# Optimization experiments

Hardware: AMD Instinct MI355X
Metric: run time of the kernel (lower is better)

The kernel has to match this reference:

```python
import jax, jax.numpy as jnp
import numpy as np

B, N, IN, H, OUT = 128, 8192, 9, 128, 9


def setup_inputs() -> dict:
    key = jax.random.key(0)
    ks = jax.random.split(key, 4)
    y = jax.random.normal(ks[0], (B, N, 6), dtype=jnp.float32)
    W1 = jax.random.normal(ks[1], (IN, H), dtype=jnp.float32) / np.sqrt(IN)
    b1 = jnp.zeros((H,), dtype=jnp.float32)
    W2 = jax.random.normal(ks[2], (H, H), dtype=jnp.float32) / np.sqrt(H)
    b2 = jnp.zeros((H,), dtype=jnp.float32)
    W3 = jax.random.normal(ks[3], (H, OUT), dtype=jnp.float32) / np.sqrt(H)
    b3 = jnp.zeros((OUT,), dtype=jnp.float32)
    return {"y": y, "W1": W1, "b1": b1, "W2": W2, "b2": b2, "W3": W3, "b3": b3}


def _make_triplets(coords):
    # coords: (B, N, 3) -> (B, N-2, 9) = (a1, a2, a3, x1, y1, x2, y2, x3, y3)
    xp = coords[:, :-2, :]
    xm = coords[:, 1:-1, :]
    xn = coords[:, 2:, :]
    off = jnp.arctan2(xm[..., 1] - xp[..., 1], xm[..., 0] - xp[..., 0])
    return jnp.stack(
        (xp[..., 2] - off, xm[..., 2] - off, xn[..., 2] - off,
         xp[..., 0], xp[..., 1], xm[..., 0], xm[..., 1], xn[..., 0], xn[..., 1]),
        axis=-1,
    )


def reference(y, W1, b1, W2, b2, W3, b3):
    coords = y[..., :3]                      # (B, N, 3)
    t = _make_triplets(coords)               # (B, N-2, 9)
    h = jax.nn.swish(t @ W1 + b1)            # (B, N-2, H)
    h = jax.nn.swish(h @ W2 + b2)            # (B, N-2, H)
    f = h @ W3 + b3                          # (B, N-2, 9)
    # overlap-add scatter back onto the N cycles
    res = jnp.zeros_like(coords)
    res = res.at[:, :-2, :].add(jnp.stack([f[..., 3], f[..., 4], f[..., 0]], axis=-1))
    res = res.at[:, 1:-1, :].add(jnp.stack([f[..., 5], f[..., 6], f[..., 1]], axis=-1))
    res = res.at[:, 2:, :].add(jnp.stack([f[..., 7], f[..., 8], f[..., 2]], axis=-1))
    # boundaries = (1, 1): clamp both ends
    res = res.at[:, 0, :].set(0.0)
    res = res.at[:, -1, :].set(0.0)
    return res
```

## Files before the change

### kernel.cpp

```cpp
#include <hip/hip_runtime.h>
#include <hip/hip_bf16.h>

#define Bn 128
#define Nn 8192
#define Hn 128
#define RPB 128
#define JOUT 126
#define NBJ 66

typedef __attribute__((ext_vector_type(8))) short short8;
typedef __attribute__((ext_vector_type(4))) float f32x4;
typedef __attribute__((ext_vector_type(4))) unsigned int u32x4;

__device__ __forceinline__ unsigned short f2bf(float x) {
    union { float f; unsigned u; } v; v.f = x;
    return (unsigned short)((v.u + 0x7fffu + ((v.u >> 16) & 1u)) >> 16);
}
__device__ __forceinline__ float bf2f(unsigned short h) {
    union { unsigned u; float f; } v; v.u = ((unsigned)h) << 16;
    return v.f;
}
__device__ __forceinline__ unsigned short flo(float x) {
    return f2bf(x - bf2f(f2bf(x)));
}
__device__ __forceinline__ float swish(float x) {
    return x * __builtin_amdgcn_rcpf(1.0f + __expf(-x));
}
__device__ __forceinline__ unsigned pk2(float a, float b) {
    union { __hip_bfloat16 h; unsigned short u; } ca, cb;
    ca.h = __float2bfloat16(a); cb.h = __float2bfloat16(b);
    return (unsigned)ca.u | ((unsigned)cb.u << 16);
}

__global__ void prep_kernel(const float* __restrict__ W1, const float* __restrict__ b1,
                            const float* __restrict__ W2, const float* __restrict__ W3,
                            unsigned short* __restrict__ ws)
{
    int tid = blockIdx.x * 256 + threadIdx.x;
    if (tid >= 22528) return;
    int f = tid >> 9, r = tid & 511;
    int l = r >> 3, e = r & 7;
    int p = ((l >> 4) << 3) | e;
    int c16 = l & 15;
    unsigned short v = 0;
    if (f < 8) {
        int col = (f << 4) | c16;
        if (p < 9)        v = f2bf(W1[p * Hn + col]);
        else if (p < 18)  v = flo(W1[(p - 9) * Hn + col]);
        else if (p < 27)  v = f2bf(W1[(p - 18) * Hn + col]);
        else if (p == 27) v = f2bf(b1[col]);
        else if (p == 28) v = flo(b1[col]);
    } else if (f < 40) {
        int mt2 = (f - 8) >> 2, ks = (f - 8) & 3;
        int col = (mt2 << 4) | c16;
        int k = 16 * (2 * ks + ((p & 7) >> 2)) + ((p >> 3) << 2) + (p & 3);
        v = f2bf(W2[k * Hn + col]);
    } else {
        int ks = f - 40;
        int k = 16 * (2 * ks + ((p & 7) >> 2)) + ((p >> 3) << 2) + (p & 3);
        if (c16 < 9) v = f2bf(W3[k * 9 + c16]);
    }
    ws[tid] = v;
}

__global__ __launch_bounds__(256, 5) void fused_kernel(
    const float* __restrict__ y, const float* __restrict__ b2g,
    const float* __restrict__ b3, const unsigned short* __restrict__ ws,
    float* __restrict__ out)
{
    __shared__ __align__(16) char tb[RPB * 80];
    __shared__ float f_lds[RPB][12];

    const int tid = threadIdx.x;
    const int lane = tid & 63;
    const int w = tid >> 6;
    const int b = blockIdx.y;
    const int j0 = blockIdx.x * JOUT;
    const int r15 = lane & 15, g = lane >> 4;

    const short8* wsf = (const short8*)ws;

    if (tid < RPB) {
        int i = j0 - 2 + tid;
        i = (i < 0) ? 0 : ((i > Nn - 3) ? (Nn - 3) : i);
        const float* base = y + ((size_t)b * Nn + i) * 6;
        float xp0 = base[0],  xp1 = base[1],  xp2 = base[2];
        float xm0 = base[6],  xm1 = base[7],  xm2 = base[8];
        float xn0 = base[12], xn1 = base[13], xn2 = base[14];
        float off = atan2f(xm1 - xp1, xm0 - xp0);
        float t0 = xp2 - off, t1 = xm2 - off, t2 = xn2 - off;
        unsigned short h0 = f2bf(t0), h1 = f2bf(t1), h2 = f2bf(t2);
        unsigned short h3 = f2bf(xp0), h4 = f2bf(xp1), h5 = f2bf(xm0);
        unsigned short h6 = f2bf(xm1), h7 = f2bf(xn0), h8 = f2bf(xn1);
        unsigned short l0 = f2bf(t0 - bf2f(h0)), l1 = f2bf(t1 - bf2f(h1));
        unsigned short l2 = f2bf(t2 - bf2f(h2)), l3 = f2bf(xp0 - bf2f(h3));
        unsigned short l4 = f2bf(xp1 - bf2f(h4)), l5 = f2bf(xm0 - bf2f(h5));
        unsigned short l6 = f2bf(xm1 - bf2f(h6)), l7 = f2bf(xn0 - bf2f(h7));
        unsigned short l8 = f2bf(xn1 - bf2f(h8));
        #define PK(a,bv) ((unsigned)(a) | ((unsigned)(bv) << 16))
        u32x4 v0 = { PK(h0,h1), PK(h2,h3), PK(h4,h5), PK(h6,h7) };
        u32x4 v1 = { PK(h8,h0), PK(h1,h2), PK(h3,h4), PK(h5,h6) };
        u32x4 v2 = { PK(h7,h8), PK(l0,l1), PK(l2,l3), PK(l4,l5) };
        u32x4 v3 = { PK(l6,l7), PK(l8,0x3F80u), PK(0x3F80u,0u), 0u };
        #undef PK
        char* dst = tb + tid * 80;
        *(u32x4*)(dst)      = v0;
        *(u32x4*)(dst + 16) = v1;
        *(u32x4*)(dst + 32) = v2;
        *(u32x4*)(dst + 48) = v3;
    }
    __syncthreads();

    short8 b2f[2][4];
    {
        short8 w1f[8];
        #pragma unroll
        for (int mt = 0; mt < 8; ++mt) w1f[mt] = wsf[mt * 64 + lane];
        #pragma unroll
        for (int nt = 0; nt < 2; ++nt) {
            short8 tf = *(const short8*)(tb + (32 * w + 16 * nt + r15) * 80 + g * 16);
            f32x4 acc1[8];
            #pragma unroll
            for (int mt = 0; mt < 8; ++mt)
                acc1[mt] = __builtin_amdgcn_mfma_f32_16x16x32_bf16(w1f[mt], tf, (f32x4)0.0f, 0, 0, 0);
            #pragma unroll
            for (int ks = 0; ks < 4; ++ks) {
                union { unsigned u[4]; short8 s; } pk;
                pk.u[0] = pk2(swish(acc1[2 * ks][0]),     swish(acc1[2 * ks][1]));
                pk.u[1] = pk2(swish(acc1[2 * ks][2]),     swish(acc1[2 * ks][3]));
                pk.u[2] = pk2(swish(acc1[2 * ks + 1][0]), swish(acc1[2 * ks + 1][1]));
                pk.u[3] = pk2(swish(acc1[2 * ks + 1][2]), swish(acc1[2 * ks + 1][3]));
                b2f[nt][ks] = pk.s;
            }
        }
    }

    f32x4 facc0 = (f32x4)0.0f, facc1 = (f32x4)0.0f;
    #pragma unroll
    for (int i = 0; i < 4; ++i) {
        unsigned cc0[4], cc1[4];
        #pragma unroll
        for (int h = 0; h < 2; ++h) {
            const int mt2 = 2 * i + h;
            short8 a0 = wsf[512 + (mt2 * 4 + 0) * 64 + lane];
            short8 a1 = wsf[512 + (mt2 * 4 + 1) * 64 + lane];
            short8 a2 = wsf[512 + (mt2 * 4 + 2) * 64 + lane];
            short8 a3 = wsf[512 + (mt2 * 4 + 3) * 64 + lane];
            const f32x4 bias = *(const f32x4*)(b2g + mt2 * 16 + 4 * g);
            #pragma unroll
            for (int nt = 0; nt < 2; ++nt) {
                f32x4 acc = __builtin_amdgcn_mfma_f32_16x16x32_bf16(a0, b2f[nt][0], (f32x4)0.0f, 0, 0, 0);
                acc = __builtin_amdgcn_mfma_f32_16x16x32_bf16(a1, b2f[nt][1], acc, 0, 0, 0);
                acc = __builtin_amdgcn_mfma_f32_16x16x32_bf16(a2, b2f[nt][2], acc, 0, 0, 0);
                acc = __builtin_amdgcn_mfma_f32_16x16x32_bf16(a3, b2f[nt][3], acc, 0, 0, 0);
                unsigned p0 = pk2(swish(acc[0] + bias[0]), swish(acc[1] + bias[1]));
                unsigned p1 = pk2(swish(acc[2] + bias[2]), swish(acc[3] + bias[3]));
                if (nt == 0) { cc0[2 * h] = p0; cc0[2 * h + 1] = p1; }
                else         { cc1[2 * h] = p0; cc1[2 * h + 1] = p1; }
            }
        }
        short8 b3fi = wsf[2560 + i * 64 + lane];
        union { unsigned u[4]; short8 s; } u0, u1;
        #pragma unroll
        for (int q = 0; q < 4; ++q) { u0.u[q] = cc0[q]; u1.u[q] = cc1[q]; }
        facc0 = __builtin_amdgcn_mfma_f32_16x16x32_bf16(u0.s, b3fi, facc0, 0, 0, 0);
        facc1 = __builtin_amdgcn_mfma_f32_16x16x32_bf16(u1.s, b3fi, facc1, 0, 0, 0);
    }

    if (r15 < 9) {
        float b3v = b3[r15];
        #pragma unroll
        for (int e = 0; e < 4; ++e) {
            f_lds[32 * w + 4 * g + e][r15]      = facc0[e] + b3v;
            f_lds[32 * w + 16 + 4 * g + e][r15] = facc1[e] + b3v;
        }
    }
    __syncthreads();

    for (int o = tid; o < 3 * JOUT; o += 256) {
        int jo = o / 3, c = o - jo * 3;
        int j = j0 + jo;
        if (j < Nn) {
            float val = 0.0f;
            if (j != 0 && j != Nn - 1) {
                int cP = (c == 0) ? 3 : (c == 1) ? 4 : 0;
                int cM = (c == 0) ? 5 : (c == 1) ? 6 : 1;
                int cN = (c == 0) ? 7 : (c == 1) ? 8 : 2;
                if (j <= Nn - 3) val += f_lds[jo + 2][cP];
                val += f_lds[jo + 1][cM];
                if (j >= 2) val += f_lds[jo][cN];
            }
            out[((size_t)b * Nn + j) * 3 + c] = val;
        }
    }
}

extern "C" void kernel_launch(void* const* d_in, const int* in_sizes, int n_in,
                              void* d_out, int out_size, void* d_ws, size_t ws_size,
                              hipStream_t stream)
{
    const float* y  = (const float*)d_in[0];
    const float* W1 = (const float*)d_in[1];
    const float* b1 = (const float*)d_in[2];
    const float* W2 = (const float*)d_in[3];
    const float* b2 = (const float*)d_in[4];
    const float* W3 = (const float*)d_in[5];
    const float* b3 = (const float*)d_in[6];
    unsigned short* ws = (unsigned short*)d_ws;
    float* out = (float*)d_out;

    prep_kernel<<<88, 256, 0, stream>>>(W1, b1, W2, W3, ws);
    dim3 grid(NBJ, Bn);
    fused_kernel<<<grid, 256, 0, stream>>>(y, b2, b3, ws, out);
}
```

Measured before the change: 100.5 us.

## Replace swish exp/rcp with packed Chebyshev polynomial and fold biases into MFMA

Swish is rewritten as max(x,0) minus a degree-11 polynomial fit of |x|·sigmoid(-|x|) over |x| in [0,8]. It is evaluated with packed two-wide float FMAs, which removes the transcendental exp and reciprocal per activation. The coefficients are computed in double precision by a single thread of the prep kernel and read from the workspace by every thread of the fused kernel. The layer-2 and layer-3 biases are now the initial MFMA accumulators, and the triplet bf16 hi/lo packing is simplified with alignbit. The costs are a constant approximation error for |x|>8 and a serial double-precision trig loop on one thread, which lengthens the prep kernel.

```diff
diff --git a/kernel.cpp b/kernel.cpp
--- a/kernel.cpp
+++ b/kernel.cpp
@@ -10,6 +10,7 @@
 
 typedef __attribute__((ext_vector_type(8))) short short8;
 typedef __attribute__((ext_vector_type(4))) float f32x4;
+typedef __attribute__((ext_vector_type(2))) float f32x2;
 typedef __attribute__((ext_vector_type(4))) unsigned int u32x4;
 
 __device__ __forceinline__ unsigned short f2bf(float x) {
@@ -23,13 +24,33 @@
 __device__ __forceinline__ unsigned short flo(float x) {
     return f2bf(x - bf2f(f2bf(x)));
 }
-__device__ __forceinline__ float swish(float x) {
-    return x * __builtin_amdgcn_rcpf(1.0f + __expf(-x));
+__device__ __forceinline__ float asf(unsigned u) {
+    union { unsigned u; float f; } v; v.u = u; return v.f;
 }
 __device__ __forceinline__ unsigned pk2(float a, float b) {
     union { __hip_bfloat16 h; unsigned short u; } ca, cb;
     ca.h = __float2bfloat16(a); cb.h = __float2bfloat16(b);
     return (unsigned)ca.u | ((unsigned)cb.u << 16);
+}
+
+struct SwCoef { float c[12]; };
+
+__device__ __forceinline__ unsigned swpk(f32x2 x, const SwCoef& C) {
+    f32x2 s;
+    s.x = __builtin_fabsf(x.x);
+    s.y = __builtin_fabsf(x.y);
+    f32x2 wv = s * 0.25f - 1.0f;
+    wv.x = fminf(wv.x, 1.0f);
+    wv.y = fminf(wv.y, 1.0f);
+    f32x2 p = { C.c[11], C.c[11] };
+    #pragma unroll
+    for (int k = 10; k >= 0; --k)
+        p = p * wv + (f32x2){ C.c[k], C.c[k] };
+    f32x2 m;
+    m.x = fmaxf(x.x, 0.0f);
+    m.y = fmaxf(x.y, 0.0f);
+    f32x2 r = m - p;
+    return pk2(r.x, r.y);
 }
 
 __global__ void prep_kernel(const float* __restrict__ W1, const float* __restrict__ b1,
@@ -61,6 +82,41 @@
         if (c16 < 9) v = f2bf(W3[k * 9 + c16]);
     }
     ws[tid] = v;
+
+    if (tid == 0) {
+        const int N = 12;
+        double F[12], th[12];
+        for (int j = 0; j < N; ++j) {
+            th[j] = 3.14159265358979323846 * (j + 0.5) / N;
+            double wv = cos(th[j]);
+            double s = 4.0 * (1.0 + wv);
+            F[j] = s / (1.0 + exp(s));
+        }
+        double Tp[12], Tc[12], Tn[12], mono[12];
+        for (int i = 0; i < N; ++i) { Tp[i] = 0; Tc[i] = 0; mono[i] = 0; }
+        for (int k = 0; k < N; ++k) {
+            double sum = 0;
+            for (int j = 0; j < N; ++j) sum += F[j] * cos((double)k * th[j]);
+            double ak = 2.0 * sum / N;
+            if (k == 0) ak *= 0.5;
+            if (k == 0) {
+                Tp[0] = 1.0;
+                mono[0] += ak;
+            } else if (k == 1) {
+                Tc[1] = 1.0;
+                mono[1] += ak;
+            } else {
+                for (int i = 0; i < N; ++i) {
+                    double lower = (i == 0) ? 0.0 : Tc[i - 1];
+                    Tn[i] = 2.0 * lower - Tp[i];
+                }
+                for (int i = 0; i < N; ++i) mono[i] += ak * Tn[i];
+                for (int i = 0; i < N; ++i) { Tp[i] = Tc[i]; Tc[i] = Tn[i]; }
+            }
+        }
+        float* cf = (float*)(ws + 22528);
+        for (int i = 0; i < N; ++i) cf[i] = (float)mono[i];
+    }
 }
 
 __global__ __launch_bounds__(256, 5) void fused_kernel(
@@ -79,6 +135,13 @@
     const int r15 = lane & 15, g = lane >> 4;
 
     const short8* wsf = (const short8*)ws;
+
+    SwCoef C;
+    {
+        const float* cf = (const float*)(ws + 22528);
+        #pragma unroll
+        for (int i = 0; i < 12; ++i) C.c[i] = cf[i];
+    }
 
     if (tid < RPB) {
         int i = j0 - 2 + tid;
@@ -89,20 +152,24 @@
         float xn0 = base[12], xn1 = base[13], xn2 = base[14];
         float off = atan2f(xm1 - xp1, xm0 - xp0);
         float t0 = xp2 - off, t1 = xm2 - off, t2 = xn2 - off;
-        unsigned short h0 = f2bf(t0), h1 = f2bf(t1), h2 = f2bf(t2);
-        unsigned short h3 = f2bf(xp0), h4 = f2bf(xp1), h5 = f2bf(xm0);
-        unsigned short h6 = f2bf(xm1), h7 = f2bf(xn0), h8 = f2bf(xn1);
-        unsigned short l0 = f2bf(t0 - bf2f(h0)), l1 = f2bf(t1 - bf2f(h1));
-        unsigned short l2 = f2bf(t2 - bf2f(h2)), l3 = f2bf(xp0 - bf2f(h3));
-        unsigned short l4 = f2bf(xp1 - bf2f(h4)), l5 = f2bf(xm0 - bf2f(h5));
-        unsigned short l6 = f2bf(xm1 - bf2f(h6)), l7 = f2bf(xn0 - bf2f(h7));
-        unsigned short l8 = f2bf(xn1 - bf2f(h8));
-        #define PK(a,bv) ((unsigned)(a) | ((unsigned)(bv) << 16))
-        u32x4 v0 = { PK(h0,h1), PK(h2,h3), PK(h4,h5), PK(h6,h7) };
-        u32x4 v1 = { PK(h8,h0), PK(h1,h2), PK(h3,h4), PK(h5,h6) };
-        u32x4 v2 = { PK(h7,h8), PK(l0,l1), PK(l2,l3), PK(l4,l5) };
-        u32x4 v3 = { PK(l6,l7), PK(l8,0x3F80u), PK(0x3F80u,0u), 0u };
-        #undef PK
+        unsigned hw0 = pk2(t0, t1);
+        unsigned hw1 = pk2(t2, xp0);
+        unsigned hw2 = pk2(xp1, xm0);
+        unsigned hw3 = pk2(xm1, xn0);
+        unsigned hw8 = pk2(xn1, 1.0f);
+        float r0 = t0  - asf(hw0 << 16), r1 = t1  - asf(hw0 & 0xffff0000u);
+        float r2 = t2  - asf(hw1 << 16), r3 = xp0 - asf(hw1 & 0xffff0000u);
+        float r4 = xp1 - asf(hw2 << 16), r5 = xm0 - asf(hw2 & 0xffff0000u);
+        float r6 = xm1 - asf(hw3 << 16), r7 = xn0 - asf(hw3 & 0xffff0000u);
+        float r8 = xn1 - asf(hw8 << 16);
+        u32x4 v0 = { hw0, hw1, hw2, hw3 };
+        u32x4 v1 = { (hw0 << 16) | (hw8 & 0xffffu),
+                     __builtin_amdgcn_alignbit(hw1, hw0, 16),
+                     __builtin_amdgcn_alignbit(hw2, hw1, 16),
+                     __builtin_amdgcn_alignbit(hw3, hw2, 16) };
+        u32x4 v2 = { __builtin_amdgcn_alignbit(hw8, hw3, 16),
+                     pk2(r0, r1), pk2(r2, r3), pk2(r4, r5) };
+        u32x4 v3 = { pk2(r6, r7), pk2(r8, 1.0f), 0x00003F80u, 0u };
         char* dst = tb + tid * 80;
         *(u32x4*)(dst)      = v0;
         *(u32x4*)(dst + 16) = v1;
@@ -126,16 +193,18 @@
             #pragma unroll
             for (int ks = 0; ks < 4; ++ks) {
                 union { unsigned u[4]; short8 s; } pk;
-                pk.u[0] = pk2(swish(acc1[2 * ks][0]),     swish(acc1[2 * ks][1]));
-                pk.u[1] = pk2(swish(acc1[2 * ks][2]),     swish(acc1[2 * ks][3]));
-                pk.u[2] = pk2(swish(acc1[2 * ks + 1][0]), swish(acc1[2 * ks + 1][1]));
-                pk.u[3] = pk2(swish(acc1[2 * ks + 1][2]), swish(acc1[2 * ks + 1][3]));
+                pk.u[0] = swpk((f32x2){acc1[2 * ks][0],     acc1[2 * ks][1]},     C);
+                pk.u[1] = swpk((f32x2){acc1[2 * ks][2],     acc1[2 * ks][3]},     C);
+                pk.u[2] = swpk((f32x2){acc1[2 * ks + 1][0], acc1[2 * ks + 1][1]}, C);
+                pk.u[3] = swpk((f32x2){acc1[2 * ks + 1][2], acc1[2 * ks + 1][3]}, C);
                 b2f[nt][ks] = pk.s;
             }
         }
     }
 
-    f32x4 facc0 = (f32x4)0.0f, facc1 = (f32x4)0.0f;
+    float b3v = (r15 < 9) ? b3[r15] : 0.0f;
+    f32x4 facc0 = { b3v, b3v, b3v, b3v };
+    f32x4 facc1 = facc0;
     #pragma unroll
     for (int i = 0; i < 4; ++i) {
         unsigned cc0[4], cc1[4];
@@ -149,12 +218,12 @@
             const f32x4 bias = *(const f32x4*)(b2g + mt2 * 16 + 4 * g);
             #pragma unroll
             for (int nt = 0; nt < 2; ++nt) {
-                f32x4 acc = __builtin_amdgcn_mfma_f32_16x16x32_bf16(a0, b2f[nt][0], (f32x4)0.0f, 0, 0, 0);
+                f32x4 acc = __builtin_amdgcn_mfma_f32_16x16x32_bf16(a0, b2f[nt][0], bias, 0, 0, 0);
                 acc = __builtin_amdgcn_mfma_f32_16x16x32_bf16(a1, b2f[nt][1], acc, 0, 0, 0);
                 acc = __builtin_amdgcn_mfma_f32_16x16x32_bf16(a2, b2f[nt][2], acc, 0, 0, 0);
                 acc = __builtin_amdgcn_mfma_f32_16x16x32_bf16(a3, b2f[nt][3], acc, 0, 0, 0);
-                unsigned p0 = pk2(swish(acc[0] + bias[0]), swish(acc[1] + bias[1]));
-                unsigned p1 = pk2(swish(acc[2] + bias[2]), swish(acc[3] + bias[3]));
+                unsigned p0 = swpk((f32x2){acc[0], acc[1]}, C);
+                unsigned p1 = swpk((f32x2){acc[2], acc[3]}, C);
                 if (nt == 0) { cc0[2 * h] = p0; cc0[2 * h + 1] = p1; }
                 else         { cc1[2 * h] = p0; cc1[2 * h + 1] = p1; }
             }
@@ -168,11 +237,10 @@
     }
 
     if (r15 < 9) {
-        float b3v = b3[r15];
         #pragma unroll
         for (int e = 0; e < 4; ++e) {
-            f_lds[32 * w + 4 * g + e][r15]      = facc0[e] + b3v;
-            f_lds[32 * w + 16 + 4 * g + e][r15] = facc1[e] + b3v;
+            f_lds[32 * w + 4 * g + e][r15]      = facc0[e];
+            f_lds[32 * w + 16 + 4 * g + e][r15] = facc1[e];
         }
     }
     __syncthreads();
```

Measured after the change: 171.0 us. 70.1% more time.
